# Kernel tuning notes

Hardware: AMD Instinct MI355X
Metric: run time of the kernel (lower is better)

The kernel has to match this reference:

```python
import jax, jax.numpy as jnp
import numpy as np

V, C, BLK = 32000, 512, 2048
B, T = 4, 2048
EPS = 1e-5


def _layernorm(x, g, b):
    mu = jnp.mean(x, axis=-1, keepdims=True)
    var = jnp.mean(jnp.square(x - mu), axis=-1, keepdims=True)
    return (x - mu) * jax.lax.rsqrt(var + EPS) * g + b


def setup_inputs() -> dict:
    key = jax.random.key(0)
    ks = jax.random.split(key, 16)
    s = 0.02
    return {
        "idx": jax.random.randint(ks[0], (B, T), 0, V),
        "targets": jax.random.randint(ks[1], (B, T), 0, V),
        "tok_emb": jax.random.normal(ks[2], (V, C), jnp.float32) * s,
        "pos_emb": jax.random.normal(ks[3], (BLK, C), jnp.float32) * s,
        "Wk": jax.random.normal(ks[4], (C, C), jnp.float32) * s,
        "Wq": jax.random.normal(ks[5], (C, C), jnp.float32) * s,
        "Wv": jax.random.normal(ks[6], (C, C), jnp.float32) * s,
        "W1": jax.random.normal(ks[7], (4 * C, C), jnp.float32) * s,
        "b1": jnp.zeros((4 * C,), jnp.float32),
        "W2": jax.random.normal(ks[8], (C, 4 * C), jnp.float32) * s,
        "b2": jnp.zeros((C,), jnp.float32),
        "g1": jnp.ones((C,), jnp.float32),
        "beta1": jnp.zeros((C,), jnp.float32),
        "g2": jnp.ones((C,), jnp.float32),
        "beta2": jnp.zeros((C,), jnp.float32),
        "Wlm": jax.random.normal(ks[9], (V, C), jnp.float32) * s,
        "blm": jnp.zeros((V,), jnp.float32),
    }


def reference(idx, targets, tok_emb, pos_emb, Wk, Wq, Wv, W1, b1, W2, b2,
              g1, beta1, g2, beta2, Wlm, blm):
    # embeddings
    x = tok_emb[idx] + pos_emb[:T]  # [B,T,C]
    # single-head causal self-attention (dropout = identity, eval mode)
    h = _layernorm(x, g1, beta1)
    q = jnp.einsum('btc,dc->btd', h, Wq)
    k = jnp.einsum('btc,dc->btd', h, Wk)
    v = jnp.einsum('btc,dc->btd', h, Wv)
    wei = jnp.einsum('btd,bsd->bts', q, k) * (C ** -0.5)  # [B,T,T]
    mask = jnp.tril(jnp.ones((T, T), bool))
    wei = jnp.where(mask, wei, -jnp.inf)
    wei = jax.nn.softmax(wei, axis=-1)
    x = x + jnp.einsum('bts,bsd->btd', wei, v)
    # FFN
    h2 = _layernorm(x, g2, beta2)
    ff = jax.nn.relu(jnp.einsum('btc,fc->btf', h2, W1) + b1)
    x = x + jnp.einsum('btf,cf->btc', ff, W2) + b2
    # lm head + cross-entropy
    logits = (jnp.einsum('btc,vc->btv', x, Wlm) + blm).reshape(B * T, V)
    logp = jax.nn.log_softmax(logits, axis=-1)
    loss = -jnp.mean(jnp.take_along_axis(logp, targets.reshape(-1, 1), axis=1))
    return logits, loss
```

## Files before the change

### kernel.cpp

```cpp
#include <hip/hip_runtime.h>

typedef __bf16 bf16;
typedef __bf16 bf16x8 __attribute__((ext_vector_type(8)));
typedef float  f32x4  __attribute__((ext_vector_type(4)));

#define NB 4
#define NT 2048
#define NC 512
#define NV 32000
#define NROWS (NB*NT)
#define NCHUNK 500
#define LNEPS 1e-5f
#define SMEM_B 131072

static __device__ __forceinline__ void load_lds16(const bf16* g, char* l) {
  __builtin_amdgcn_global_load_lds(
      (const __attribute__((address_space(1))) void*)g,
      (__attribute__((address_space(3))) void*)l, 16, 0, 0);
}

static __device__ __forceinline__ void bar() {
  asm volatile("" ::: "memory");
  __builtin_amdgcn_s_barrier();
  asm volatile("" ::: "memory");
}

__global__ __launch_bounds__(256)
void cvt_kernel(const float* __restrict__ in, bf16* __restrict__ out, int n8) {
  long i = (long)blockIdx.x * 256 + threadIdx.x;
  long stride = (long)gridDim.x * 256;
  for (; i < n8; i += stride) {
    const float* p = in + i * 8;
    f32x4 a = *(const f32x4*)p;
    f32x4 b = *(const f32x4*)(p + 4);
    bf16x8 o;
    o[0]=(bf16)a.x; o[1]=(bf16)a.y; o[2]=(bf16)a.z; o[3]=(bf16)a.w;
    o[4]=(bf16)b.x; o[5]=(bf16)b.y; o[6]=(bf16)b.z; o[7]=(bf16)b.w;
    *(bf16x8*)(out + i*8) = o;
  }
}

__global__ __launch_bounds__(64)
void embed_ln_kernel(const int* __restrict__ idx, const float* __restrict__ tok,
                     const float* __restrict__ pos, const float* __restrict__ gw,
                     const float* __restrict__ bw,
                     float* __restrict__ x0, bf16* __restrict__ h1) {
  int row = blockIdx.x;
  int t = row & (NT-1);
  int id = idx[row];
  int lane = threadIdx.x;
  const float* tr = tok + (long)id*NC + lane*8;
  const float* pr = pos + (long)t*NC + lane*8;
  f32x4 a0 = *(const f32x4*)tr, a1 = *(const f32x4*)(tr+4);
  f32x4 p0 = *(const f32x4*)pr, p1 = *(const f32x4*)(pr+4);
  f32x4 r0 = a0 + p0, r1 = a1 + p1;
  float* o = x0 + (long)row*NC + lane*8;
  *(f32x4*)o = r0; *(f32x4*)(o+4) = r1;
  float v[8] = {r0.x,r0.y,r0.z,r0.w,r1.x,r1.y,r1.z,r1.w};
  float s = 0.f;
  #pragma unroll
  for (int j=0;j<8;++j) s += v[j];
  #pragma unroll
  for (int m=32;m>=1;m>>=1) s += __shfl_xor(s, m);
  float mu = s * (1.f/NC);
  float sq = 0.f;
  #pragma unroll
  for (int j=0;j<8;++j) { v[j] -= mu; sq += v[j]*v[j]; }
  #pragma unroll
  for (int m=32;m>=1;m>>=1) sq += __shfl_xor(sq, m);
  float rs = rsqrtf(sq * (1.f/NC) + LNEPS);
  const float* gp = gw + lane*8;
  const float* bp = bw + lane*8;
  f32x4 g0 = *(const f32x4*)gp, g1 = *(const f32x4*)(gp+4);
  f32x4 b0 = *(const f32x4*)bp, b1 = *(const f32x4*)(bp+4);
  float gg[8] = {g0.x,g0.y,g0.z,g0.w,g1.x,g1.y,g1.z,g1.w};
  float bb[8] = {b0.x,b0.y,b0.z,b0.w,b1.x,b1.y,b1.z,b1.w};
  bf16x8 oo;
  #pragma unroll
  for (int j=0;j<8;++j) oo[j] = (bf16)(v[j]*rs*gg[j] + bb[j]);
  *(bf16x8*)(h1 + (long)row*NC + lane*8) = oo;
}

__global__ __launch_bounds__(256)
void transpose_kernel(const bf16* __restrict__ v, long ldv, bf16* __restrict__ vt) {
  __shared__ bf16 tile[64][66];
  int b = blockIdx.z;
  int t0 = blockIdx.x*64, c0 = blockIdx.y*64;
  int tid = threadIdx.x;
  int r = tid >> 2, ch = (tid & 3) * 16;
  const bf16* src = v + ((long)b*NT + t0 + r)*ldv + c0 + ch;
  #pragma unroll
  for (int i=0;i<16;++i) tile[r][ch+i] = src[i];
  __syncthreads();
  bf16x8 o0, o1;
  #pragma unroll
  for (int i=0;i<8;++i) o0[i] = tile[ch+i][r];
  #pragma unroll
  for (int i=0;i<8;++i) o1[i] = tile[ch+8+i][r];
  bf16* dst = vt + ((long)b*NC + c0 + r)*NT + t0 + ch;
  *(bf16x8*)dst = o0;
  *(bf16x8*)(dst+8) = o1;
}

__global__ __launch_bounds__(256)
void softmax_kernel(float* __restrict__ S) {
  const int row = blockIdx.x;
  const int t = row & (NT-1);
  const int tid = threadIdx.x;
  float* sr = S + (long)row*NT;
  bf16* pr = (bf16*)S + (long)row*(2*NT);
  const float scale = 0.044194173824159216f;
  f32x4 v0 = *(const f32x4*)(sr + tid*8);
  f32x4 v1 = *(const f32x4*)(sr + tid*8 + 4);
  float v[8] = {v0.x,v0.y,v0.z,v0.w,v1.x,v1.y,v1.z,v1.w};
  int cb = tid*8;
  float mx = -1e30f;
  #pragma unroll
  for (int j=0;j<8;++j) {
    v[j] = (cb + j <= t) ? v[j]*scale : -1e30f;
    mx = fmaxf(mx, v[j]);
  }
  __shared__ float redm[4];
  #pragma unroll
  for (int m=32;m>=1;m>>=1) mx = fmaxf(mx, __shfl_xor(mx, m));
  if ((tid & 63) == 0) redm[tid>>6] = mx;
  __syncthreads();
  mx = fmaxf(fmaxf(redm[0],redm[1]), fmaxf(redm[2],redm[3]));
  float e[8]; float s = 0.f;
  #pragma unroll
  for (int j=0;j<8;++j) { e[j] = (cb + j <= t) ? __expf(v[j]-mx) : 0.f; s += e[j]; }
  __shared__ float reds[4];
  #pragma unroll
  for (int m=32;m>=1;m>>=1) s += __shfl_xor(s, m);
  if ((tid & 63) == 0) reds[tid>>6] = s;
  __syncthreads();
  s = reds[0]+reds[1]+reds[2]+reds[3];
  float inv = 1.f/s;
  bf16x8 o;
  #pragma unroll
  for (int j=0;j<8;++j) o[j] = (bf16)(e[j]*inv);
  *(bf16x8*)(pr + cb) = o;
}

enum { EPI_F32=0, EPI_BF16=1, EPI_BIAS_RELU_BF16=2, EPI_BIAS_RES_BF16=3, EPI_RES_F32=4 };

template<int EPI, bool CAUSAL=false, bool SWAP=false, bool KCHUNK=false>
__global__ __launch_bounds__(512,2)
void gemm256(const bf16* __restrict__ A, const bf16* __restrict__ B, int nkt,
             long lda, long ldb, long sAb, long sBb,
             float* __restrict__ outf, bf16* __restrict__ outb, long ldo, long sOb,
             const float* __restrict__ bias,
             const float* __restrict__ res, long ldr, long sRb) {
  extern __shared__ char smem[];
  int bn, bm;
  if constexpr (SWAP) { bm = blockIdx.x; bn = blockIdx.y; }
  else               { bn = blockIdx.x; bm = blockIdx.y; }
  const int bz = blockIdx.z;
  if constexpr (CAUSAL) { if (bn > bm) return; }
  int nkt_eff = nkt;
  int bzAB = bz;
  long kOff = 0;
  if constexpr (KCHUNK) {
    int c = bz >> 2; bzAB = bz & 3;
    int lim = (bm+1)*4 - c*8;
    if (lim <= 0) return;
    if (lim < nkt_eff) nkt_eff = lim;
    kOff = (long)c*512;
  }

  const int tid = threadIdx.x;
  const int wid = tid >> 6, lane = tid & 63;
  const int wr = wid >> 2, wc = wid & 3;
  const int l15 = lane & 15, g = lane >> 4;

  const bf16* Ab = A + (long)bzAB*sAb + kOff + (long)bm*256*lda;
  const bf16* Bb = B + (long)bzAB*sBb + kOff + (long)bn*256*ldb;

  const int colsw = 8 * ((tid & 7) ^ ((tid >> 3) & 7));
  const bf16* A0 = Ab + (long)(tid >> 3)*lda + colsw;
  const bf16* B0 = Bb + (long)(tid >> 3)*ldb + colsw;

  auto stage = [&](int ab, int t, int h, int slot) {
    char* dst = smem + slot*65536 + ab*32768 + h*16384 + wid*1024;
    const bf16* s0 = (ab ? B0 : A0) + (long)(h*128)*(ab ? ldb : lda) + (long)t*64;
    load_lds16(s0, dst);
    load_lds16(s0 + 64*(ab ? ldb : lda), dst + 8192);
  };

  const char* sm = smem;
  auto aLoad = [&](int slot, int m, int kk) -> bf16x8 {
    int row = m*16 + l15;
    int b = row*128 + ((kk*64 + g*16) ^ ((row & 7) << 4));
    return *(const bf16x8*)(sm + slot*65536 + wr*16384 + b);
  };
  auto bLoad = [&](int slot, int n, int kk) -> bf16x8 {
    int row = (wc & 1)*64 + n*16 + l15;
    int b = row*128 + ((kk*64 + g*16) ^ ((row & 7) << 4));
    return *(const bf16x8*)(sm + slot*65536 + 32768 + (wc >> 1)*16384 + b);
  };

  f32x4 acc[8][4] = {};

  stage(0, 0, 0, 0);
  stage(0, 0, 1, 0);
  stage(1, 0, 0, 0);
  stage(1, 0, 1, 0);
  stage(0, 1, 0, 1);
  asm volatile("s_waitcnt vmcnt(2)" ::: "memory");
  bar();

  const int niter = nkt_eff >> 1;
  for (int it = 0; it < niter; ++it) {
    const int t0 = 2*it, t1 = 2*it + 1;
    const int tn0 = (t0+2 < nkt_eff) ? t0+2 : nkt_eff-1;
    const int tn1 = (t1+2 < nkt_eff) ? t1+2 : nkt_eff-1;
    bf16x8 a0[4][2], a1[4][2], b0[2][2], b1[2][2];

    #pragma unroll
    for (int m=0;m<4;++m) { a0[m][0]=aLoad(0,m,0); a0[m][1]=aLoad(0,m,1); }
    #pragma unroll
    for (int n=0;n<2;++n) { b0[n][0]=bLoad(0,n,0); b0[n][1]=bLoad(0,n,1); }
    stage(0, t1, 1, 1);
    bar();
    __builtin_amdgcn_s_setprio(1);
    #pragma unroll
    for (int m=0;m<4;++m)
      #pragma unroll
      for (int n=0;n<2;++n) {
        acc[m][n] = __builtin_amdgcn_mfma_f32_16x16x32_bf16(a0[m][0], b0[n][0], acc[m][n],0,0,0);
        acc[m][n] = __builtin_amdgcn_mfma_f32_16x16x32_bf16(a0[m][1], b0[n][1], acc[m][n],0,0,0);
      }
    __builtin_amdgcn_s_setprio(0);
    bar();
    #pragma unroll
    for (int n=0;n<2;++n) { b1[n][0]=bLoad(0,n+2,0); b1[n][1]=bLoad(0,n+2,1); }
    stage(1, t1, 0, 1);
    bar();
    __builtin_amdgcn_s_setprio(1);
    #pragma unroll
    for (int m=0;m<4;++m)
      #pragma unroll
      for (int n=0;n<2;++n) {
        acc[m][n+2] = __builtin_amdgcn_mfma_f32_16x16x32_bf16(a0[m][0], b1[n][0], acc[m][n+2],0,0,0);
        acc[m][n+2] = __builtin_amdgcn_mfma_f32_16x16x32_bf16(a0[m][1], b1[n][1], acc[m][n+2],0,0,0);
      }
    __builtin_amdgcn_s_setprio(0);
    bar();
    #pragma unroll
    for (int m=0;m<4;++m) { a1[m][0]=aLoad(0,m+4,0); a1[m][1]=aLoad(0,m+4,1); }
    stage(1, t1, 1, 1);
    bar();
    __builtin_amdgcn_s_setprio(1);
    #pragma unroll
    for (int m=0;m<4;++m)
      #pragma unroll
      for (int n=0;n<2;++n) {
        acc[m+4][n+2] = __builtin_amdgcn_mfma_f32_16x16x32_bf16(a1[m][0], b1[n][0], acc[m+4][n+2],0,0,0);
        acc[m+4][n+2] = __builtin_amdgcn_mfma_f32_16x16x32_bf16(a1[m][1], b1[n][1], acc[m+4][n+2],0,0,0);
      }
    __builtin_amdgcn_s_setprio(0);
    bar();
    stage(0, tn0, 0, 0);
    asm volatile("s_waitcnt vmcnt(2)" ::: "memory");
    bar();
    __builtin_amdgcn_s_setprio(1);
    #pragma unroll
    for (int m=0;m<4;++m)
      #pragma unroll
      for (int n=0;n<2;++n) {
        acc[m+4][n] = __builtin_amdgcn_mfma_f32_16x16x32_bf16(a1[m][0], b0[n][0], acc[m+4][n],0,0,0);
        acc[m+4][n] = __builtin_amdgcn_mfma_f32_16x16x32_bf16(a1[m][1], b0[n][1], acc[m+4][n],0,0,0);
      }
    __builtin_amdgcn_s_setprio(0);
    bar();
    #pragma unroll
    for (int m=0;m<4;++m) { a0[m][0]=aLoad(1,m,0); a0[m][1]=aLoad(1,m,1); }
    #pragma unroll
    for (int n=0;n<2;++n) { b0[n][0]=bLoad(1,n,0); b0[n][1]=bLoad(1,n,1); }
    stage(0, tn0, 1, 0);
    bar();
    __builtin_amdgcn_s_setprio(1);
    #pragma unroll
    for (int m=0;m<4;++m)
      #pragma unroll
      for (int n=0;n<2;++n) {
        acc[m][n] = __builtin_amdgcn_mfma_f32_16x16x32_bf16(a0[m][0], b0[n][0], acc[m][n],0,0,0);
        acc[m][n] = __builtin_amdgcn_mfma_f32_16x16x32_bf16(a0[m][1], b0[n][1], acc[m][n],0,0,0);
      }
    __builtin_amdgcn_s_setprio(0);
    bar();
    #pragma unroll
    for (int n=0;n<2;++n) { b1[n][0]=bLoad(1,n+2,0); b1[n][1]=bLoad(1,n+2,1); }
    stage(1, tn0, 0, 0);
    bar();
    __builtin_amdgcn_s_setprio(1);
    #pragma unroll
    for (int m=0;m<4;++m)
      #pragma unroll
      for (int n=0;n<2;++n) {
        acc[m][n+2] = __builtin_amdgcn_mfma_f32_16x16x32_bf16(a0[m][0], b1[n][0], acc[m][n+2],0,0,0);
        acc[m][n+2] = __builtin_amdgcn_mfma_f32_16x16x32_bf16(a0[m][1], b1[n][1], acc[m][n+2],0,0,0);
      }
    __builtin_amdgcn_s_setprio(0);
    bar();
    #pragma unroll
    for (int m=0;m<4;++m) { a1[m][0]=aLoad(1,m+4,0); a1[m][1]=aLoad(1,m+4,1); }
    stage(1, tn0, 1, 0);
    bar();
    __builtin_amdgcn_s_setprio(1);
    #pragma unroll
    for (int m=0;m<4;++m)
      #pragma unroll
      for (int n=0;n<2;++n) {
        acc[m+4][n+2] = __builtin_amdgcn_mfma_f32_16x16x32_bf16(a1[m][0], b1[n][0], acc[m+4][n+2],0,0,0);
        acc[m+4][n+2] = __builtin_amdgcn_mfma_f32_16x16x32_bf16(a1[m][1], b1[n][1], acc[m+4][n+2],0,0,0);
      }
    __builtin_amdgcn_s_setprio(0);
    bar();
    stage(0, tn1, 0, 1);
    asm volatile("s_waitcnt vmcnt(2)" ::: "memory");
    bar();
    __builtin_amdgcn_s_setprio(1);
    #pragma unroll
    for (int m=0;m<4;++m)
      #pragma unroll
      for (int n=0;n<2;++n) {
        acc[m+4][n] = __builtin_amdgcn_mfma_f32_16x16x32_bf16(a1[m][0], b0[n][0], acc[m+4][n],0,0,0);
        acc[m+4][n] = __builtin_amdgcn_mfma_f32_16x16x32_bf16(a1[m][1], b0[n][1], acc[m+4][n],0,0,0);
      }
    __builtin_amdgcn_s_setprio(0);
    bar();
  }

  const long rowbase = (long)bm*256 + wr*128;
  const long colbase = (long)bn*256 + wc*64;

  #pragma unroll
  for (int m=0;m<8;++m)
    #pragma unroll
    for (int n=0;n<4;++n) {
      long c = colbase + n*16 + l15;
      #pragma unroll
      for (int q_=0;q_<4;++q_) {
        long rr = rowbase + m*16 + g*4 + q_;
        float v = acc[m][n][q_];
        if constexpr (EPI == EPI_F32) {
          outf[(long)bz*sOb + rr*ldo + c] = v;
        } else if constexpr (EPI == EPI_BF16) {
          outb[(long)bz*sOb + rr*ldo + c] = (bf16)v;
        } else if constexpr (EPI == EPI_BIAS_RELU_BF16) {
          outb[rr*ldo + c] = (bf16)fmaxf(v + bias[c], 0.f);
        } else if constexpr (EPI == EPI_BIAS_RES_BF16) {
          outb[rr*ldo + c] = (bf16)(v + bias[c] + res[rr*ldr + c]);
        } else if constexpr (EPI == EPI_RES_F32) {
          outf[(long)bz*sOb + rr*ldo + c] = v + res[(long)bz*sRb + rr*ldr + c];
        }
      }
    }
}

__global__ __launch_bounds__(256,4)
void lmhead128(const bf16* __restrict__ A, const bf16* __restrict__ B,
               const float* __restrict__ bias, float* __restrict__ outf,
               float* __restrict__ pmax, float* __restrict__ psum) {
  __shared__ char sm[32768];
  const int bm = blockIdx.x, bn = blockIdx.y;
  const int tid = threadIdx.x;
  const int wid = tid >> 6, lane = tid & 63;
  const int wr = wid >> 1, wc = wid & 1;
  const int l15 = lane & 15, g = lane >> 4;

  const int p0 = tid, p1 = tid + 256;
  const int r0_ = 2*(p0>>3) + ((p0>>2)&1), c0_ = 8*((p0&3) ^ ((p0>>3)&3));
  const int r1_ = 2*(p1>>3) + ((p1>>2)&1), c1_ = 8*((p1&3) ^ ((p1>>3)&3));
  const bf16* A00 = A + ((long)bm*128 + r0_)*NC + c0_;
  const bf16* A01 = A + ((long)bm*128 + r1_)*NC + c1_;
  const bf16* B00 = B + ((long)bn*128 + r0_)*NC + c0_;
  const bf16* B01 = B + ((long)bn*128 + r1_)*NC + c1_;

  auto stage = [&](int kt, int slot) {
    char* base = sm + slot*16384 + wid*1024;
    load_lds16(A00 + kt*32, base);
    load_lds16(A01 + kt*32, base + 4096);
    load_lds16(B00 + kt*32, base + 8192);
    load_lds16(B01 + kt*32, base + 12288);
  };

  auto aLoad = [&](int slot, int m) -> bf16x8 {
    int R = wr*64 + m*16 + l15;
    return *(const bf16x8*)(sm + slot*16384 + (R>>1)*128 + (R&1)*64
                            + ((g ^ ((R>>1)&3)) << 4));
  };
  auto bLoad = [&](int slot, int n) -> bf16x8 {
    int R = wc*64 + n*16 + l15;
    return *(const bf16x8*)(sm + slot*16384 + 8192 + (R>>1)*128 + (R&1)*64
                            + ((g ^ ((R>>1)&3)) << 4));
  };

  f32x4 acc[4][4] = {};

  stage(0, 0);
  asm volatile("s_waitcnt vmcnt(0)" ::: "memory");
  bar();

  int cur = 0;
  for (int kt = 0; kt < 16; ++kt) {
    if (kt < 15) stage(kt + 1, cur ^ 1);
    bf16x8 af[4], bf_[4];
    #pragma unroll
    for (int m=0;m<4;++m) af[m] = aLoad(cur, m);
    #pragma unroll
    for (int n=0;n<4;++n) bf_[n] = bLoad(cur, n);
    __builtin_amdgcn_s_setprio(1);
    #pragma unroll
    for (int m=0;m<4;++m)
      #pragma unroll
      for (int n=0;n<4;++n)
        acc[m][n] = __builtin_amdgcn_mfma_f32_16x16x32_bf16(af[m], bf_[n], acc[m][n],0,0,0);
    __builtin_amdgcn_s_setprio(0);
    asm volatile("s_waitcnt vmcnt(0)" ::: "memory");
    bar();
    cur ^= 1;
  }

  const long rowb = (long)bm*128;
  const long colb = (long)bn*128;
  #pragma unroll
  for (int n=0;n<4;++n) {
    float bv = bias[colb + wc*64 + n*16 + l15];
    #pragma unroll
    for (int m=0;m<4;++m)
      #pragma unroll
      for (int q=0;q<4;++q) acc[m][n][q] += bv;
  }
  #pragma unroll
  for (int m=0;m<4;++m)
    #pragma unroll
    for (int q=0;q<4;++q) {
      float mx = fmaxf(fmaxf(acc[m][0][q], acc[m][1][q]),
                       fmaxf(acc[m][2][q], acc[m][3][q]));
      #pragma unroll
      for (int msk=8;msk>=1;msk>>=1) mx = fmaxf(mx, __shfl_xor(mx, msk));
      float se = 0.f;
      #pragma unroll
      for (int n=0;n<4;++n) se += __expf(acc[m][n][q] - mx);
      #pragma unroll
      for (int msk=8;msk>=1;msk>>=1) se += __shfl_xor(se, msk);
      if (l15 == 0) {
        long row = rowb + wr*64 + m*16 + g*4 + q;
        pmax[row*NCHUNK + bn*2 + wc] = mx;
        psum[row*NCHUNK + bn*2 + wc] = se;
      }
    }
  float* lbuf = (float*)(sm + wid*4096);
  #pragma unroll
  for (int m=0;m<4;++m) {
    #pragma unroll
    for (int n=0;n<4;++n)
      #pragma unroll
      for (int q=0;q<4;++q)
        lbuf[(g*4+q)*64 + n*16 + l15] = acc[m][n][q];
    #pragma unroll
    for (int p=0;p<4;++p) {
      f32x4 v = *(const f32x4*)&lbuf[(p*4+g)*64 + l15*4];
      long row = rowb + wr*64 + m*16 + p*4 + g;
      long col = colb + wc*64 + l15*4;
      __builtin_nontemporal_store(v, (f32x4*)&outf[row*NV + col]);
    }
  }
}

__global__ __launch_bounds__(64)
void pv_combine_ln_kernel(const float* __restrict__ part, const float* __restrict__ x0,
                          const float* __restrict__ gw, const float* __restrict__ bw,
                          float* __restrict__ x1, bf16* __restrict__ h2) {
  int row = blockIdx.x;
  int b = row >> 11, t = row & (NT-1);
  int lane = threadIdx.x;
  int nC = (t >> 9) + 1;
  const float* xr = x0 + (long)row*NC + lane*8;
  f32x4 a0 = *(const f32x4*)xr, a1 = *(const f32x4*)(xr+4);
  for (int c = 0; c < nC; ++c) {
    const float* pr = part + ((long)(c*4 + b)*NT + t)*NC + lane*8;
    a0 += *(const f32x4*)pr; a1 += *(const f32x4*)(pr+4);
  }
  float* o = x1 + (long)row*NC + lane*8;
  *(f32x4*)o = a0; *(f32x4*)(o+4) = a1;
  float v[8] = {a0.x,a0.y,a0.z,a0.w,a1.x,a1.y,a1.z,a1.w};
  float s = 0.f;
  #pragma unroll
  for (int j=0;j<8;++j) s += v[j];
  #pragma unroll
  for (int m=32;m>=1;m>>=1) s += __shfl_xor(s, m);
  float mu = s * (1.f/NC);
  float sq = 0.f;
  #pragma unroll
  for (int j=0;j<8;++j) { v[j] -= mu; sq += v[j]*v[j]; }
  #pragma unroll
  for (int m=32;m>=1;m>>=1) sq += __shfl_xor(sq, m);
  float rs = rsqrtf(sq * (1.f/NC) + LNEPS);
  const float* gp = gw + lane*8;
  const float* bp = bw + lane*8;
  f32x4 g0 = *(const f32x4*)gp, g1 = *(const f32x4*)(gp+4);
  f32x4 b0 = *(const f32x4*)bp, b1 = *(const f32x4*)(bp+4);
  float gg[8] = {g0.x,g0.y,g0.z,g0.w,g1.x,g1.y,g1.z,g1.w};
  float bb[8] = {b0.x,b0.y,b0.z,b0.w,b1.x,b1.y,b1.z,b1.w};
  bf16x8 oo;
  #pragma unroll
  for (int j=0;j<8;++j) oo[j] = (bf16)(v[j]*rs*gg[j] + bb[j]);
  *(bf16x8*)(h2 + (long)row*NC + lane*8) = oo;
}

__global__ __launch_bounds__(64)
void ffn2_combine_kernel(const float* __restrict__ part, const float* __restrict__ x1,
                         const float* __restrict__ b2, bf16* __restrict__ x2) {
  int row = blockIdx.x;
  int lane = threadIdx.x;
  const float* xr = x1 + (long)row*NC + lane*8;
  f32x4 a0 = *(const f32x4*)xr, a1 = *(const f32x4*)(xr+4);
  const float* br = b2 + lane*8;
  a0 += *(const f32x4*)br; a1 += *(const f32x4*)(br+4);
  #pragma unroll
  for (int z = 0; z < 4; ++z) {
    const float* pr = part + ((long)z*NROWS + row)*NC + lane*8;
    a0 += *(const f32x4*)pr; a1 += *(const f32x4*)(pr+4);
  }
  bf16x8 o;
  o[0]=(bf16)a0.x; o[1]=(bf16)a0.y; o[2]=(bf16)a0.z; o[3]=(bf16)a0.w;
  o[4]=(bf16)a1.x; o[5]=(bf16)a1.y; o[6]=(bf16)a1.z; o[7]=(bf16)a1.w;
  *(bf16x8*)(x2 + (long)row*NC + lane*8) = o;
}

__global__ __launch_bounds__(512)
void loss1_kernel(const float* __restrict__ pmax, const float* __restrict__ psum,
                  const float* __restrict__ logits, const int* __restrict__ targets,
                  float* __restrict__ rowloss) {
  int row = blockIdx.x;
  int tid = threadIdx.x;
  int lane = tid & 63, wv = tid >> 6;
  float cm = (tid < NCHUNK) ? pmax[(long)row*NCHUNK + tid] : -1e30f;
  float cs = (tid < NCHUNK) ? psum[(long)row*NCHUNK + tid] : 0.f;
  float mx = cm;
  #pragma unroll
  for (int m=32;m>=1;m>>=1) mx = fmaxf(mx, __shfl_xor(mx, m));
  __shared__ float rm[8];
  if (lane == 0) rm[wv] = mx;
  __syncthreads();
  float M = rm[0];
  #pragma unroll
  for (int i=1;i<8;++i) M = fmaxf(M, rm[i]);
  float sc = cs * __expf(cm - M);
  #pragma unroll
  for (int m=32;m>=1;m>>=1) sc += __shfl_xor(sc, m);
  __shared__ float rs_[8];
  if (lane == 0) rs_[wv] = sc;
  __syncthreads();
  if (tid == 0) {
    float Sv = 0.f;
    #pragma unroll
    for (int i=0;i<8;++i) Sv += rs_[i];
    float lse = M + logf(Sv);
    int tgt = targets[row];
    float lg = logits[(long)row*NV + tgt];
    rowloss[row] = lse - lg;
  }
}

__global__ __launch_bounds__(256)
void loss2_kernel(const float* __restrict__ rowloss, float* __restrict__ out) {
  int tid = threadIdx.x;
  float s = 0.f;
  for (int i = tid; i < NROWS; i += 256) s += rowloss[i];
  #pragma unroll
  for (int m=32;m>=1;m>>=1) s += __shfl_xor(s, m);
  __shared__ float rs_[4];
  if ((tid & 63) == 0) rs_[tid>>6] = s;
  __syncthreads();
  if (tid == 0) out[0] = (rs_[0]+rs_[1]+rs_[2]+rs_[3]) * (1.f/NROWS);
}

extern "C" void kernel_launch(void* const* d_in, const int* in_sizes, int n_in,
                              void* d_out, int out_size, void* d_ws, size_t ws_size,
                              hipStream_t stream) {
  const int*   idx  = (const int*)d_in[0];
  const int*   tgt  = (const int*)d_in[1];
  const float* tok  = (const float*)d_in[2];
  const float* pos  = (const float*)d_in[3];
  const float* Wk   = (const float*)d_in[4];
  const float* Wq   = (const float*)d_in[5];
  const float* Wv   = (const float*)d_in[6];
  const float* W1   = (const float*)d_in[7];
  const float* b1   = (const float*)d_in[8];
  const float* W2   = (const float*)d_in[9];
  const float* b2   = (const float*)d_in[10];
  const float* g1   = (const float*)d_in[11];
  const float* be1  = (const float*)d_in[12];
  const float* g2   = (const float*)d_in[13];
  const float* be2  = (const float*)d_in[14];
  const float* Wlm  = (const float*)d_in[15];
  const float* blm  = (const float*)d_in[16];

  float* logits = (float*)d_out;
  float* loss   = logits + (long)NROWS*NV;

  char* w = (char*)d_ws;
  auto alloc = [&](size_t bytes) -> char* {
    char* p = w; w += (bytes + 255) & ~(size_t)255; return p;
  };
  bf16* wqkvb = (bf16*)alloc((size_t)3*NC*NC*2);
  bf16* w1b   = (bf16*)alloc((size_t)4*NC*NC*2);
  bf16* w2b   = (bf16*)alloc((size_t)4*NC*NC*2);
  bf16* wlmb  = (bf16*)alloc((size_t)NV*NC*2);
  float* x0   = (float*)alloc((size_t)NROWS*NC*4);
  bf16* h1b   = (bf16*)alloc((size_t)NROWS*NC*2);
  bf16* qkvb  = (bf16*)alloc((size_t)NROWS*3*NC*2);
  bf16* vtb   = (bf16*)alloc((size_t)NROWS*NC*2);
  float* Sb   = (float*)alloc((size_t)NB*NT*NT*4);
  float* pvp  = (float*)alloc((size_t)16*NT*NC*4);
  float* x1   = (float*)alloc((size_t)NROWS*NC*4);
  bf16* h2b   = (bf16*)alloc((size_t)NROWS*NC*2);
  bf16* ffb   = (bf16*)alloc((size_t)NROWS*4*NC*2);
  bf16* x2b   = (bf16*)alloc((size_t)NROWS*NC*2);
  float* pmax = (float*)alloc((size_t)NROWS*NCHUNK*4);
  float* psum = (float*)alloc((size_t)NROWS*NCHUNK*4);
  float* rowloss = (float*)alloc((size_t)NROWS*4);
  float* ff2p = Sb;

  hipFuncSetAttribute((const void*)gemm256<EPI_BF16,false,false,false>,
                      hipFuncAttributeMaxDynamicSharedMemorySize, SMEM_B);
  hipFuncSetAttribute((const void*)gemm256<EPI_F32,true,false,false>,
                      hipFuncAttributeMaxDynamicSharedMemorySize, SMEM_B);
  hipFuncSetAttribute((const void*)gemm256<EPI_F32,false,false,true>,
                      hipFuncAttributeMaxDynamicSharedMemorySize, SMEM_B);
  hipFuncSetAttribute((const void*)gemm256<EPI_F32,false,false,false>,
                      hipFuncAttributeMaxDynamicSharedMemorySize, SMEM_B);
  hipFuncSetAttribute((const void*)gemm256<EPI_BIAS_RELU_BF16,false,true,false>,
                      hipFuncAttributeMaxDynamicSharedMemorySize, SMEM_B);

  auto cvt = [&](const float* in, bf16* out, long n) {
    int n8 = (int)(n/8);
    int blocks = (n8 + 255)/256; if (blocks > 2048) blocks = 2048;
    cvt_kernel<<<blocks, 256, 0, stream>>>(in, out, n8);
  };
  cvt(Wq, wqkvb, (long)NC*NC);
  cvt(Wk, wqkvb + (long)NC*NC, (long)NC*NC);
  cvt(Wv, wqkvb + (long)2*NC*NC, (long)NC*NC);
  cvt(W1, w1b, (long)4*NC*NC);
  cvt(W2, w2b, (long)4*NC*NC);
  cvt(Wlm, wlmb, (long)NV*NC);

  embed_ln_kernel<<<NROWS, 64, 0, stream>>>(idx, tok, pos, g1, be1, x0, h1b);

  gemm256<EPI_BF16><<<dim3(6,32,1), 512, SMEM_B, stream>>>(
      h1b, wqkvb, 8, NC, NC, 0, 0, nullptr, qkvb, 3*NC, 0,
      nullptr, nullptr, 0, 0);

  transpose_kernel<<<dim3(NT/64, NC/64, NB), 256, 0, stream>>>(qkvb + 2*NC, 3*NC, vtb);

  gemm256<EPI_F32,true><<<dim3(8,8,NB), 512, SMEM_B, stream>>>(
      qkvb, qkvb + NC, 8, 3*NC, 3*NC, (long)NT*3*NC, (long)NT*3*NC,
      Sb, nullptr, NT, (long)NT*NT,
      nullptr, nullptr, 0, 0);

  softmax_kernel<<<NROWS, 256, 0, stream>>>(Sb);

  gemm256<EPI_F32,false,false,true><<<dim3(2,8,16), 512, SMEM_B, stream>>>(
      (const bf16*)Sb, vtb, 8, 2*NT, NT, (long)NT*2*NT, (long)NC*NT,
      pvp, nullptr, NC, (long)NT*NC,
      nullptr, nullptr, 0, 0);

  pv_combine_ln_kernel<<<NROWS, 64, 0, stream>>>(pvp, x0, g2, be2, x1, h2b);

  gemm256<EPI_BIAS_RELU_BF16,false,true><<<dim3(32,8,1), 512, SMEM_B, stream>>>(
      h2b, w1b, 8, NC, NC, 0, 0, nullptr, ffb, 4*NC, 0,
      b1, nullptr, 0, 0);

  gemm256<EPI_F32><<<dim3(2,32,4), 512, SMEM_B, stream>>>(
      ffb, w2b, 8, 4*NC, 4*NC, 512, 512,
      ff2p, nullptr, NC, (long)NROWS*NC,
      nullptr, nullptr, 0, 0);

  ffn2_combine_kernel<<<NROWS, 64, 0, stream>>>(ff2p, x1, b2, x2b);

  lmhead128<<<dim3(64, NV/128), 256, 0, stream>>>(x2b, wlmb, blm, logits, pmax, psum);

  loss1_kernel<<<NROWS, 512, 0, stream>>>(pmax, psum, logits, tgt, rowloss);
  loss2_kernel<<<1, 256, 0, stream>>>(rowloss, loss);
}
```

Before: 722.7 us.

## Pre-pack LM head operands into MFMA fragment layout and drop LDS staging

The LM head weights and the final activations are now written in a fragment-major bf16 layout that matches the 16x16x32 MFMA operand order. The LM head kernel then loads each operand fragment straight from global memory into registers. This removes the LDS double-buffer and the barriers, and each wave computes its own 64x64 tile. In exchange there is no LDS reuse within the block, so operand traffic relies on L2/MALL caching, and global loads are no longer overlapped with MFMA through explicit prefetch.

```diff
diff --git a/kernel.cpp b/kernel.cpp
--- a/kernel.cpp
+++ b/kernel.cpp
@@ -37,6 +37,24 @@
     o[0]=(bf16)a.x; o[1]=(bf16)a.y; o[2]=(bf16)a.z; o[3]=(bf16)a.w;
     o[4]=(bf16)b.x; o[5]=(bf16)b.y; o[6]=(bf16)b.z; o[7]=(bf16)b.w;
     *(bf16x8*)(out + i*8) = o;
+  }
+}
+
+__global__ __launch_bounds__(256)
+void cvt_pack_kernel(const float* __restrict__ in, bf16* __restrict__ out, long nfrag) {
+  long t = (long)blockIdx.x * 256 + threadIdx.x;
+  long stride = (long)gridDim.x * 256;
+  for (; t < nfrag * 64; t += stride) {
+    long f = t >> 6; int lane = (int)(t & 63);
+    long r16 = f >> 4; int ks = (int)(f & 15);
+    long row = r16 * 16 + (lane & 15);
+    int col = ks * 32 + (lane >> 4) * 8;
+    const float* p = in + row * NC + col;
+    f32x4 x = *(const f32x4*)p, y = *(const f32x4*)(p + 4);
+    bf16x8 o;
+    o[0]=(bf16)x.x; o[1]=(bf16)x.y; o[2]=(bf16)x.z; o[3]=(bf16)x.w;
+    o[4]=(bf16)y.x; o[5]=(bf16)y.y; o[6]=(bf16)y.z; o[7]=(bf16)y.w;
+    *(bf16x8*)((char*)out + f * 1024 + (long)lane * 16) = o;
   }
 }
 
@@ -360,74 +378,39 @@
 }
 
 __global__ __launch_bounds__(256,4)
-void lmhead128(const bf16* __restrict__ A, const bf16* __restrict__ B,
-               const float* __restrict__ bias, float* __restrict__ outf,
-               float* __restrict__ pmax, float* __restrict__ psum) {
-  __shared__ char sm[32768];
-  const int bm = blockIdx.x, bn = blockIdx.y;
+void lmheadD(const bf16* __restrict__ pA, const bf16* __restrict__ pB,
+             const float* __restrict__ bias, float* __restrict__ outf,
+             float* __restrict__ pmax, float* __restrict__ psum) {
+  __shared__ char sm[16384];
   const int tid = threadIdx.x;
-  const int wid = tid >> 6, lane = tid & 63;
-  const int wr = wid >> 1, wc = wid & 1;
+  const int wave = tid >> 6, lane = tid & 63;
   const int l15 = lane & 15, g = lane >> 4;
-
-  const int p0 = tid, p1 = tid + 256;
-  const int r0_ = 2*(p0>>3) + ((p0>>2)&1), c0_ = 8*((p0&3) ^ ((p0>>3)&3));
-  const int r1_ = 2*(p1>>3) + ((p1>>2)&1), c1_ = 8*((p1&3) ^ ((p1>>3)&3));
-  const bf16* A00 = A + ((long)bm*128 + r0_)*NC + c0_;
-  const bf16* A01 = A + ((long)bm*128 + r1_)*NC + c1_;
-  const bf16* B00 = B + ((long)bn*128 + r0_)*NC + c0_;
-  const bf16* B01 = B + ((long)bn*128 + r1_)*NC + c1_;
-
-  auto stage = [&](int kt, int slot) {
-    char* base = sm + slot*16384 + wid*1024;
-    load_lds16(A00 + kt*32, base);
-    load_lds16(A01 + kt*32, base + 4096);
-    load_lds16(B00 + kt*32, base + 8192);
-    load_lds16(B01 + kt*32, base + 12288);
-  };
-
-  auto aLoad = [&](int slot, int m) -> bf16x8 {
-    int R = wr*64 + m*16 + l15;
-    return *(const bf16x8*)(sm + slot*16384 + (R>>1)*128 + (R&1)*64
-                            + ((g ^ ((R>>1)&3)) << 4));
-  };
-  auto bLoad = [&](int slot, int n) -> bf16x8 {
-    int R = wc*64 + n*16 + l15;
-    return *(const bf16x8*)(sm + slot*16384 + 8192 + (R>>1)*128 + (R&1)*64
-                            + ((g ^ ((R>>1)&3)) << 4));
-  };
+  const int bm  = blockIdx.x * 16 + (blockIdx.y & 15);
+  const int bnt = (blockIdx.y >> 4) * 4 + wave;
+
+  const char* Ab = (const char*)pA + (long)bm*64*1024 + (long)lane*16;
+  const char* Bb = (const char*)pB + (long)bnt*64*1024 + (long)lane*16;
 
   f32x4 acc[4][4] = {};
 
-  stage(0, 0);
-  asm volatile("s_waitcnt vmcnt(0)" ::: "memory");
-  bar();
-
-  int cur = 0;
-  for (int kt = 0; kt < 16; ++kt) {
-    if (kt < 15) stage(kt + 1, cur ^ 1);
-    bf16x8 af[4], bf_[4];
-    #pragma unroll
-    for (int m=0;m<4;++m) af[m] = aLoad(cur, m);
-    #pragma unroll
-    for (int n=0;n<4;++n) bf_[n] = bLoad(cur, n);
-    __builtin_amdgcn_s_setprio(1);
+  for (int ks = 0; ks < 16; ++ks) {
+    bf16x8 a[4], b[4];
+    #pragma unroll
+    for (int m=0;m<4;++m) a[m] = *(const bf16x8*)(Ab + (long)(m*16 + ks)*1024);
+    #pragma unroll
+    for (int n=0;n<4;++n) b[n] = *(const bf16x8*)(Bb + (long)(n*16 + ks)*1024);
     #pragma unroll
     for (int m=0;m<4;++m)
       #pragma unroll
       for (int n=0;n<4;++n)
-        acc[m][n] = __builtin_amdgcn_mfma_f32_16x16x32_bf16(af[m], bf_[n], acc[m][n],0,0,0);
-    __builtin_amdgcn_s_setprio(0);
-    asm volatile("s_waitcnt vmcnt(0)" ::: "memory");
-    bar();
-    cur ^= 1;
-  }
-
-  const long rowb = (long)bm*128;
-  const long colb = (long)bn*128;
+        acc[m][n] = __builtin_amdgcn_mfma_f32_16x16x32_bf16(a[m], b[n], acc[m][n],0,0,0);
+  }
+
+  const long rowb = (long)bm*64;
+  const long colb = (long)bnt*64;
   #pragma unroll
   for (int n=0;n<4;++n) {
-    float bv = bias[colb + wc*64 + n*16 + l15];
+    float bv = bias[colb + n*16 + l15];
     #pragma unroll
     for (int m=0;m<4;++m)
       #pragma unroll
@@ -447,12 +430,12 @@
       #pragma unroll
       for (int msk=8;msk>=1;msk>>=1) se += __shfl_xor(se, msk);
       if (l15 == 0) {
-        long row = rowb + wr*64 + m*16 + g*4 + q;
-        pmax[row*NCHUNK + bn*2 + wc] = mx;
-        psum[row*NCHUNK + bn*2 + wc] = se;
+        long row = rowb + m*16 + g*4 + q;
+        pmax[row*NCHUNK + bnt] = mx;
+        psum[row*NCHUNK + bnt] = se;
       }
     }
-  float* lbuf = (float*)(sm + wid*4096);
+  float* lbuf = (float*)(sm + wave*4096);
   #pragma unroll
   for (int m=0;m<4;++m) {
     #pragma unroll
@@ -463,8 +446,8 @@
     #pragma unroll
     for (int p=0;p<4;++p) {
       f32x4 v = *(const f32x4*)&lbuf[(p*4+g)*64 + l15*4];
-      long row = rowb + wr*64 + m*16 + p*4 + g;
-      long col = colb + wc*64 + l15*4;
+      long row = rowb + m*16 + p*4 + g;
+      long col = colb + l15*4;
       __builtin_nontemporal_store(v, (f32x4*)&outf[row*NV + col]);
     }
   }
@@ -513,22 +496,25 @@
 
 __global__ __launch_bounds__(64)
 void ffn2_combine_kernel(const float* __restrict__ part, const float* __restrict__ x1,
-                         const float* __restrict__ b2, bf16* __restrict__ x2) {
+                         const float* __restrict__ b2, bf16* __restrict__ x2p) {
   int row = blockIdx.x;
-  int lane = threadIdx.x;
-  const float* xr = x1 + (long)row*NC + lane*8;
+  int ln = threadIdx.x;
+  const float* xr = x1 + (long)row*NC + ln*8;
   f32x4 a0 = *(const f32x4*)xr, a1 = *(const f32x4*)(xr+4);
-  const float* br = b2 + lane*8;
+  const float* br = b2 + ln*8;
   a0 += *(const f32x4*)br; a1 += *(const f32x4*)(br+4);
   #pragma unroll
   for (int z = 0; z < 4; ++z) {
-    const float* pr = part + ((long)z*NROWS + row)*NC + lane*8;
+    const float* pr = part + ((long)z*NROWS + row)*NC + ln*8;
     a0 += *(const f32x4*)pr; a1 += *(const f32x4*)(pr+4);
   }
   bf16x8 o;
   o[0]=(bf16)a0.x; o[1]=(bf16)a0.y; o[2]=(bf16)a0.z; o[3]=(bf16)a0.w;
   o[4]=(bf16)a1.x; o[5]=(bf16)a1.y; o[6]=(bf16)a1.z; o[7]=(bf16)a1.w;
-  *(bf16x8*)(x2 + (long)row*NC + lane*8) = o;
+  int ks = ln >> 2, g = ln & 3;
+  long frag = (long)(row >> 4)*16 + ks;
+  int laneif = g*16 + (row & 15);
+  *(bf16x8*)((char*)x2p + frag*1024 + (long)laneif*16) = o;
 }
 
 __global__ __launch_bounds__(512)
@@ -620,7 +606,7 @@
   float* x1   = (float*)alloc((size_t)NROWS*NC*4);
   bf16* h2b   = (bf16*)alloc((size_t)NROWS*NC*2);
   bf16* ffb   = (bf16*)alloc((size_t)NROWS*4*NC*2);
-  bf16* x2b   = (bf16*)alloc((size_t)NROWS*NC*2);
+  bf16* x2p   = (bf16*)alloc((size_t)NROWS*NC*2);
   float* pmax = (float*)alloc((size_t)NROWS*NCHUNK*4);
   float* psum = (float*)alloc((size_t)NROWS*NCHUNK*4);
   float* rowloss = (float*)alloc((size_t)NROWS*4);
@@ -647,7 +633,7 @@
   cvt(Wv, wqkvb + (long)2*NC*NC, (long)NC*NC);
   cvt(W1, w1b, (long)4*NC*NC);
   cvt(W2, w2b, (long)4*NC*NC);
-  cvt(Wlm, wlmb, (long)NV*NC);
+  cvt_pack_kernel<<<2048, 256, 0, stream>>>(Wlm, wlmb, (long)(NV/16)*16);
 
   embed_ln_kernel<<<NROWS, 64, 0, stream>>>(idx, tok, pos, g1, be1, x0, h1b);
 
@@ -680,9 +666,9 @@
       ff2p, nullptr, NC, (long)NROWS*NC,
       nullptr, nullptr, 0, 0);
 
-  ffn2_combine_kernel<<<NROWS, 64, 0, stream>>>(ff2p, x1, b2, x2b);
-
-  lmhead128<<<dim3(64, NV/128), 256, 0, stream>>>(x2b, wlmb, blm, logits, pmax, psum);
+  ffn2_combine_kernel<<<NROWS, 64, 0, stream>>>(ff2p, x1, b2, x2p);
+
+  lmheadD<<<dim3(8, 2000), 256, 0, stream>>>(x2p, wlmb, blm, logits, pmax, psum);
 
   loss1_kernel<<<NROWS, 512, 0, stream>>>(pmax, psum, logits, tgt, rowloss);
   loss2_kernel<<<1, 256, 0, stream>>>(rowloss, loss);
```

Result: slower. 844.4 us (+16.8%).
